# Performance work log

Measured on AMD Instinct MI355X. Metric: run time of the kernel, lower is better.

The kernel has to match this reference:

```python
import jax, jax.numpy as jnp
import numpy as np

N0, D, H, E0 = 50000, 128, 128, 800000
N1, E1, A, B, C = 20000, 320000, 100000, 64, 10


def _gcn(x, row, col, ew, n, W, b):
    # GCNConv: out = D^-1/2 (A + I) D^-1/2 (x W) + b, with edge weights
    xw = x @ W
    sl = jnp.arange(n)
    r = jnp.concatenate([row, sl])
    c = jnp.concatenate([col, sl])
    w = jnp.concatenate([ew, jnp.ones((n,), ew.dtype)])
    deg = jax.ops.segment_sum(w, c, num_segments=n)
    dinv = jax.lax.rsqrt(jnp.maximum(deg, 1e-12))
    norm = dinv[r] * w * dinv[c]
    return jax.ops.segment_sum(norm[:, None] * xw[r], c, num_segments=n) + b


def _block(x, row, col, ew, n, W1, b1, W2, b2, Wl, bl):
    # Block with num_inner_layers=2, jumping_knowledge='cat'
    x1 = jax.nn.relu(_gcn(x, row, col, ew, n, W1, b1))
    x2 = jax.nn.relu(_gcn(x1, row, col, ew, n, W2, b2))
    return jnp.concatenate([x1, x2], axis=1) @ Wl + bl


def _seg_max(x, idx, n):
    m = jax.ops.segment_max(x, idx, num_segments=n)
    return jnp.where(jnp.isfinite(m), m, 0.0)  # empty segments -> 0 like scatter_max default


def _lin_init(k, i, o):
    s = 1.0 / np.sqrt(i)
    return jax.random.uniform(k, (i, o), jnp.float32, -s, s)


def setup_inputs() -> dict:
    key = jax.random.key(0)
    ks = jax.random.split(key, 20)
    x = jax.random.normal(ks[0], (N0, D), jnp.float32)
    edge_index0 = jax.random.randint(ks[1], (2, E0), 0, N0)
    edge_weight0 = jax.random.uniform(ks[2], (E0,), jnp.float32)
    batch0 = jnp.sort(jax.random.randint(ks[3], (N0,), 0, B))
    cover_row = jax.random.randint(ks[4], (A,), 0, N0)
    cover_col = jnp.concatenate([jnp.arange(N1), jax.random.randint(ks[5], (A - N1,), 0, N1)])
    edge_index1 = jax.random.randint(ks[6], (2, E1), 0, N1)
    edge_weight1 = jax.random.uniform(ks[7], (E1,), jnp.float32)
    batch1 = jnp.sort(jax.random.randint(ks[8], (N1,), 0, B))
    params = dict(
        w_in1=_lin_init(ks[9], D, H), b_in1=jnp.zeros((H,), jnp.float32),
        w_in2=_lin_init(ks[10], H, H), b_in2=jnp.zeros((H,), jnp.float32),
        w_in_lin=_lin_init(ks[11], 2 * H, H), b_in_lin=jnp.zeros((H,), jnp.float32),
        w_b1=_lin_init(ks[12], 2 * H, H), b_b1=jnp.zeros((H,), jnp.float32),
        w_b2=_lin_init(ks[13], H, H), b_b2=jnp.zeros((H,), jnp.float32),
        w_b_lin=_lin_init(ks[14], 2 * H, H), b_b_lin=jnp.zeros((H,), jnp.float32),
        bn_gamma=jnp.ones((4 * H,), jnp.float32), bn_beta=jnp.zeros((4 * H,), jnp.float32),
        w_l1=_lin_init(ks[15], 4 * H, H), b_l1=jnp.zeros((H,), jnp.float32),
        w_l2=_lin_init(ks[16], H, C), b_l2=jnp.zeros((C,), jnp.float32),
    )
    return dict(x=x, edge_index0=edge_index0, edge_weight0=edge_weight0, batch0=batch0,
                cover_row=cover_row, cover_col=cover_col, edge_index1=edge_index1,
                edge_weight1=edge_weight1, batch1=batch1, **params)


def reference(x, edge_index0, edge_weight0, batch0, cover_row, cover_col,
              edge_index1, edge_weight1, batch1,
              w_in1, b_in1, w_in2, b_in2, w_in_lin, b_in_lin,
              w_b1, b_b1, w_b2, b_b2, w_b_lin, b_b_lin,
              bn_gamma, bn_beta, w_l1, b_l1, w_l2, b_l2):
    r0, c0 = edge_index0[0], edge_index0[1]
    h = jax.nn.relu(_block(x, r0, c0, edge_weight0, N0, w_in1, b_in1, w_in2, b_in2, w_in_lin, b_in_lin))
    xs = [jax.ops.segment_sum(h, batch0, num_segments=B), _seg_max(h, batch0, B)]
    # cover_pool_node: add + max over k-plex cover assignments
    hg = h[cover_row]
    h2 = jnp.concatenate([jax.ops.segment_sum(hg, cover_col, num_segments=N1),
                          _seg_max(hg, cover_col, N1)], axis=1)
    r1, c1 = edge_index1[0], edge_index1[1]
    h2 = jax.nn.relu(_block(h2, r1, c1, edge_weight1, N1, w_b1, b_b1, w_b2, b_b2, w_b_lin, b_b_lin))
    xs.append(jax.ops.segment_sum(h2, batch1, num_segments=B))
    xs.append(_seg_max(h2, batch1, B))
    z = jnp.concatenate(xs, axis=1)  # [B, 4H]
    # BatchNorm1d in eval mode: running stats (mean=0, var=1), eps=1e-5
    z = z * (bn_gamma * jax.lax.rsqrt(jnp.asarray(1.0 + 1e-5, z.dtype))) + bn_beta
    z = jax.nn.relu(z @ w_l1 + b_l1)
    logits = z @ w_l2 + b_l2  # dropout skipped (eval mode)
    return jax.nn.softmax(logits, axis=-1)
```

## Files before the change

### kernel.cpp

```cpp
#include <hip/hip_runtime.h>
#include <cmath>

#define HF 128
#define EPB 2048

namespace {

typedef __attribute__((ext_vector_type(8))) short short8;
typedef __attribute__((ext_vector_type(4))) float f32x4;

inline int cdiv(int a, int b) { return (a + b - 1) / b; }

__device__ inline unsigned short f2bf(float x) {
    unsigned u = __float_as_uint(x);
    return (unsigned short)((u + 0x7fffu + ((u >> 16) & 1u)) >> 16);
}
__device__ inline float bf2f(unsigned short u) {
    return __uint_as_float((unsigned)u << 16);
}
__device__ inline float bflo(unsigned v) { return __uint_as_float(v << 16); }
__device__ inline float bfhi(unsigned v) { return __uint_as_float(v & 0xffff0000u); }

#define FIXS 4194304.0f
#define FIXINV 2.384185791015625e-07f
#define SUMMASK ((1ULL << 40) - 1)

template <int K, bool AF32>
__device__ __forceinline__ void gemm_dev(int bid, const void* __restrict__ A1v, int lda1,
                                         const void* __restrict__ A2v, int lda2,
                                         const unsigned short* __restrict__ wpk,
                                         const float* __restrict__ bias, int relu,
                                         unsigned short* __restrict__ out, int N) {
    const int t = threadIdx.x;
    const int wv = t >> 6, lane = t & 63;
    const int l15 = lane & 15, lhi = lane >> 4;
    const int rbase = bid * 128 + wv * 32;

    f32x4 acc[2][8];
#pragma unroll
    for (int i = 0; i < 2; ++i)
#pragma unroll
        for (int g = 0; g < 8; ++g) acc[i][g] = {0.f, 0.f, 0.f, 0.f};

    int r[2];
#pragma unroll
    for (int ri = 0; ri < 2; ++ri) {
        int rr = rbase + ri * 16 + l15;
        r[ri] = (rr < N) ? rr : (N - 1);
    }

    for (int kc = 0; kc < K / 32; ++kc) {
        int kb = kc * 32 + lhi * 8;
        short8 a[2];
#pragma unroll
        for (int ri = 0; ri < 2; ++ri) {
            if (AF32) {
                const float* A = (const float*)A1v;
                const float* p = A + (size_t)r[ri] * lda1 + kb;
                float4 f0 = *reinterpret_cast<const float4*>(p);
                float4 f1 = *reinterpret_cast<const float4*>(p + 4);
                a[ri][0] = (short)f2bf(f0.x); a[ri][1] = (short)f2bf(f0.y);
                a[ri][2] = (short)f2bf(f0.z); a[ri][3] = (short)f2bf(f0.w);
                a[ri][4] = (short)f2bf(f1.x); a[ri][5] = (short)f2bf(f1.y);
                a[ri][6] = (short)f2bf(f1.z); a[ri][7] = (short)f2bf(f1.w);
            } else {
                const unsigned short* base;
                int kk, ld;
                if (K == 256 && kb >= 128) { base = (const unsigned short*)A2v; kk = kb - 128; ld = lda2; }
                else                       { base = (const unsigned short*)A1v; kk = kb;       ld = lda1; }
                a[ri] = *reinterpret_cast<const short8*>(base + (size_t)r[ri] * ld + kk);
            }
        }
        const unsigned short* wb = wpk + (size_t)(kc * 8) * 512 + lane * 8;
#pragma unroll
        for (int g = 0; g < 8; ++g) {
            short8 b = *reinterpret_cast<const short8*>(wb + (size_t)g * 512);
            acc[0][g] = __builtin_amdgcn_mfma_f32_16x16x32_bf16(a[0], b, acc[0][g], 0, 0, 0);
            acc[1][g] = __builtin_amdgcn_mfma_f32_16x16x32_bf16(a[1], b, acc[1][g], 0, 0, 0);
        }
    }

#pragma unroll
    for (int ri = 0; ri < 2; ++ri) {
#pragma unroll
        for (int g = 0; g < 8; ++g) {
            int col = l15 + g * 16;
            float bb = bias ? bias[col] : 0.f;
#pragma unroll
            for (int e = 0; e < 4; ++e) {
                int rr = rbase + ri * 16 + lhi * 4 + e;
                if (rr < N) {
                    float v = acc[ri][g][e] + bb;
                    if (relu) v = fmaxf(v, 0.f);
                    out[(size_t)rr * 128 + col] = f2bf(v);
                }
            }
        }
    }
}

template <int K, bool AF32>
__global__ void k_mfma_gemm(const void* __restrict__ A1v, int lda1,
                            const void* __restrict__ A2v, int lda2,
                            const unsigned short* __restrict__ wpk,
                            const float* __restrict__ bias, int relu,
                            unsigned short* __restrict__ out, int N) {
    gemm_dev<K, AF32>(blockIdx.x, A1v, lda1, A2v, lda2, wpk, bias, relu, out, N);
}

__device__ __forceinline__ void hist_dev(int e, int E, const int* __restrict__ col,
                                         const float* __restrict__ ew,
                                         unsigned long long* __restrict__ dc,
                                         unsigned* __restrict__ rank) {
    if (e < E) {
        unsigned long long v = (1ULL << 40) | (unsigned long long)(ew[e] * FIXS + 0.5f);
        unsigned long long old = atomicAdd(&dc[col[e]], v);
        rank[e] = (unsigned)(old >> 40);
    }
}

__device__ inline void scan256(int* s, int v, int gid, int n, int* __restrict__ excl,
                               int* __restrict__ partial, int pb) {
    s[threadIdx.x] = v;
    __syncthreads();
    for (int off = 1; off < 256; off <<= 1) {
        int t = (threadIdx.x >= off) ? s[threadIdx.x - off] : 0;
        __syncthreads();
        s[threadIdx.x] += t;
        __syncthreads();
    }
    if (gid < n) excl[gid] = s[threadIdx.x] - v;
    if (threadIdx.x == 255) partial[pb] = s[255];
}

__device__ __forceinline__ void fill_dev(int b, int t, const int* __restrict__ row,
                                         const int* __restrict__ col, const float* __restrict__ ew,
                                         const unsigned* __restrict__ rank,
                                         const float* __restrict__ dinv, const int* __restrict__ rp,
                                         int2* __restrict__ ed, int E, int Nn) {
    int xcd = b & 7, chunk = b >> 3;
    int lo = (int)((long long)Nn * xcd >> 3), hi = (int)((long long)Nn * (xcd + 1) >> 3);
    int base = chunk * EPB;
#pragma unroll
    for (int i = 0; i < EPB; i += 256) {
        int e = base + i + t;
        if (e < E) {
            int c = col[e];
            if (c >= lo && c < hi) {
                int r = row[e];
                ed[rp[c] + rank[e]] = make_int2(r, __float_as_int(ew[e] * dinv[r] * dinv[c]));
            }
        }
    }
}

__device__ __forceinline__ void gather_dev(int b, const unsigned* __restrict__ xw, int n,
                                           const int* __restrict__ rp, const int2* __restrict__ ed,
                                           const float* __restrict__ dinv,
                                           const float* __restrict__ bias,
                                           unsigned* __restrict__ out) {
    int wid = (b * 256 + (int)threadIdx.x) >> 6;
    if (wid >= n) return;
    int lane = threadIdx.x & 63;
    int s = rp[wid], e = rp[wid + 1];
    float d = dinv[wid];
    unsigned v = xw[(size_t)wid * 64 + lane];
    float ax = bflo(v) * d * d, ay = bfhi(v) * d * d;
    float bx = 0.f, by = 0.f, cx = 0.f, cy = 0.f, dx = 0.f, dy = 0.f;
    int i = s;
    for (; i + 4 <= e; i += 4) {
        unsigned long long p0 = __builtin_nontemporal_load((const unsigned long long*)(ed + i));
        unsigned long long p1 = __builtin_nontemporal_load((const unsigned long long*)(ed + i + 1));
        unsigned long long p2 = __builtin_nontemporal_load((const unsigned long long*)(ed + i + 2));
        unsigned long long p3 = __builtin_nontemporal_load((const unsigned long long*)(ed + i + 3));
        unsigned v0 = xw[(size_t)(unsigned)(p0 & 0xffffffffu) * 64 + lane];
        unsigned v1 = xw[(size_t)(unsigned)(p1 & 0xffffffffu) * 64 + lane];
        unsigned v2 = xw[(size_t)(unsigned)(p2 & 0xffffffffu) * 64 + lane];
        unsigned v3 = xw[(size_t)(unsigned)(p3 & 0xffffffffu) * 64 + lane];
        float c0 = __uint_as_float((unsigned)(p0 >> 32));
        float c1 = __uint_as_float((unsigned)(p1 >> 32));
        float c2 = __uint_as_float((unsigned)(p2 >> 32));
        float c3 = __uint_as_float((unsigned)(p3 >> 32));
        ax += c0 * bflo(v0); ay += c0 * bfhi(v0);
        bx += c1 * bflo(v1); by += c1 * bfhi(v1);
        cx += c2 * bflo(v2); cy += c2 * bfhi(v2);
        dx += c3 * bflo(v3); dy += c3 * bfhi(v3);
    }
    for (; i < e; ++i) {
        unsigned long long p0 = __builtin_nontemporal_load((const unsigned long long*)(ed + i));
        unsigned v0 = xw[(size_t)(unsigned)(p0 & 0xffffffffu) * 64 + lane];
        float c0 = __uint_as_float((unsigned)(p0 >> 32));
        ax += c0 * bflo(v0); ay += c0 * bfhi(v0);
    }
    ax += bx + cx + dx;
    ay += by + cy + dy;
    float2 bb = *reinterpret_cast<const float2*>(bias + lane * 2);
    ax = fmaxf(ax + bb.x, 0.f);
    ay = fmaxf(ay + bb.y, 0.f);
    out[(size_t)wid * 64 + lane] = (unsigned)f2bf(ax) | ((unsigned)f2bf(ay) << 16);
}

__global__ void k_prep0(const float* __restrict__ w0, const float* __restrict__ w1,
                        const float* __restrict__ w2, const float* __restrict__ w3,
                        const float* __restrict__ w4, const float* __restrict__ w5,
                        unsigned short* __restrict__ wpk,
                        const int* __restrict__ b0, int n0, const int* __restrict__ b1,
                        int n1, int B, int* __restrict__ bst0, int* __restrict__ bst1) {
    int b = blockIdx.x, t = threadIdx.x;
    if (b < 576) {
        int idx = b * 256 + t;
        const float* src; int local;
        if      (idx < 16384)  { src = w0; local = idx; }
        else if (idx < 32768)  { src = w1; local = idx - 16384; }
        else if (idx < 65536)  { src = w2; local = idx - 32768; }
        else if (idx < 98304)  { src = w3; local = idx - 65536; }
        else if (idx < 114688) { src = w4; local = idx - 98304; }
        else                   { src = w5; local = idx - 114688; }
        int e = local & 7, lane = (local >> 3) & 63, g = (local >> 9) & 7, kc = local >> 12;
        int colw = (lane & 15) + 16 * g;
        int k = kc * 32 + ((lane >> 4) << 3) + e;
        wpk[idx] = f2bf(src[k * 128 + colw]);
        return;
    }
    int idx = t;
    if (idx < 2 * (B + 1)) {
        int which = idx > B;
        int bb = which ? idx - (B + 1) : idx;
        const int* arr = which ? b1 : b0;
        int lo = 0, hi = which ? n1 : n0;
        while (lo < hi) {
            int mid = (lo + hi) >> 1;
            if (arr[mid] < bb) lo = mid + 1; else hi = mid;
        }
        (which ? bst1 : bst0)[bb] = lo;
    }
}

__global__ void k_prep1(const float* __restrict__ x, const unsigned short* __restrict__ wpk,
                        unsigned short* __restrict__ xw, int N0gemm, int nbG,
                        const int* __restrict__ col0, const float* __restrict__ ew0,
                        unsigned long long* __restrict__ dc0, unsigned* __restrict__ rank0,
                        int E0) {
    int b = blockIdx.x;
    if (b < nbG) {
        gemm_dev<128, true>(b, x, 128, nullptr, 0, wpk, nullptr, 0, xw, N0gemm);
        return;
    }
    b -= nbG;
    hist_dev(b * 256 + (int)threadIdx.x, E0, col0, ew0, dc0, rank0);
}

__global__ void k_scanA(const unsigned long long* __restrict__ dc0, int* __restrict__ rp0,
                        int* __restrict__ part0, float* __restrict__ dinv0, int n0) {
    __shared__ int s[256];
    int gid = blockIdx.x * 256 + threadIdx.x;
    int v = (gid < n0) ? (int)(dc0[gid] >> 40) : 0;
    scan256(s, v, gid, n0, rp0, part0, blockIdx.x);
    if (gid < n0) dinv0[gid] = rsqrtf(1.0f + (float)(dc0[gid] & SUMMASK) * FIXINV);
}

__global__ void k_scan2a(int* __restrict__ p0, int nb0) {
    __shared__ int s[256];
    int v = (threadIdx.x < nb0) ? p0[threadIdx.x] : 0;
    s[threadIdx.x] = v;
    __syncthreads();
    for (int off = 1; off < 256; off <<= 1) {
        int t = (threadIdx.x >= off) ? s[threadIdx.x - off] : 0;
        __syncthreads();
        s[threadIdx.x] += t;
        __syncthreads();
    }
    if (threadIdx.x < nb0) p0[threadIdx.x] = s[threadIdx.x] - v;
}

__global__ void k_scan3a(int* __restrict__ rp0, const int* __restrict__ part0, int n0, int tot) {
    int gid = blockIdx.x * 256 + threadIdx.x;
    if (gid < n0) rp0[gid] += part0[blockIdx.x];
    if (gid == 0) rp0[n0] = tot;
}

__global__ void k_fill0(const int* __restrict__ row0, const int* __restrict__ col0,
                        const float* __restrict__ ew0, const unsigned* __restrict__ rank0,
                        const float* __restrict__ dinv0, const int* __restrict__ rp0,
                        int2* __restrict__ ed0, int E0, int N0n) {
    fill_dev(blockIdx.x, threadIdx.x, row0, col0, ew0, rank0, dinv0, rp0, ed0, E0, N0n);
}

__global__ void k_gather_hist(const unsigned* __restrict__ xw, int n,
                              const int* __restrict__ rp, const int2* __restrict__ ed,
                              const float* __restrict__ dinv, const float* __restrict__ bias,
                              unsigned* __restrict__ out, int G,
                              const int* __restrict__ col1, const float* __restrict__ ew1,
                              unsigned long long* __restrict__ dc1, unsigned* __restrict__ rank1,
                              int E1, int nb1,
                              const int* __restrict__ ccol, int* __restrict__ ccnt,
                              unsigned* __restrict__ rankc, int A) {
    int b = blockIdx.x;
    if (b < G) { gather_dev(b, xw, n, rp, ed, dinv, bias, out); return; }
    b -= G;
    int t = threadIdx.x;
    if (b < nb1) { hist_dev(b * 256 + t, E1, col1, ew1, dc1, rank1); return; }
    b -= nb1;
    int e = b * 256 + t;
    if (e < A) rankc[e] = (unsigned)atomicAdd(&ccnt[ccol[e]], 1);
}

__global__ void k_gemm_scan(const void* __restrict__ A1v, const unsigned short* __restrict__ wpk,
                            unsigned short* __restrict__ out, int N, int nbG,
                            const unsigned long long* __restrict__ dc1, int* __restrict__ rp1,
                            int* __restrict__ part1, float* __restrict__ dinv1, int n1, int nbs1,
                            const int* __restrict__ ccnt, int* __restrict__ crp,
                            int* __restrict__ cpart, int nc) {
    __shared__ int s[256];
    int b = blockIdx.x;
    if (b < nbG) {
        gemm_dev<128, false>(b, A1v, 128, nullptr, 0, wpk, nullptr, 0, out, N);
        return;
    }
    b -= nbG;
    if (b < nbs1) {
        int gid = b * 256 + threadIdx.x;
        int v = (gid < n1) ? (int)(dc1[gid] >> 40) : 0;
        scan256(s, v, gid, n1, rp1, part1, b);
        if (gid < n1) dinv1[gid] = rsqrtf(1.0f + (float)(dc1[gid] & SUMMASK) * FIXINV);
        return;
    }
    b -= nbs1;
    {
        int gid = b * 256 + threadIdx.x;
        int v = (gid < nc) ? ccnt[gid] : 0;
        scan256(s, v, gid, nc, crp, cpart, b);
    }
}

__global__ void k_scan2b(int* __restrict__ p1, int nb1, int* __restrict__ p2, int nb2) {
    __shared__ int s[256];
    int* p = (blockIdx.x == 0) ? p1 : p2;
    int nb = (blockIdx.x == 0) ? nb1 : nb2;
    int v = (threadIdx.x < nb) ? p[threadIdx.x] : 0;
    s[threadIdx.x] = v;
    __syncthreads();
    for (int off = 1; off < 256; off <<= 1) {
        int t = (threadIdx.x >= off) ? s[threadIdx.x - off] : 0;
        __syncthreads();
        s[threadIdx.x] += t;
        __syncthreads();
    }
    if (threadIdx.x < nb) p[threadIdx.x] = s[threadIdx.x] - v;
}

__global__ void k_scan3b(int* __restrict__ rp1, const int* __restrict__ part1, int n1, int tot1,
                         int nb1, int* __restrict__ crp, const int* __restrict__ cpart,
                         int nc, int totc) {
    int b = blockIdx.x, t = threadIdx.x;
    if (b < nb1) {
        int gid = b * 256 + t;
        if (gid < n1) rp1[gid] += part1[b];
        if (gid == 0) rp1[n1] = tot1;
        return;
    }
    b -= nb1;
    int gid = b * 256 + t;
    if (gid < nc) crp[gid] += cpart[b];
    if (gid == 0) crp[nc] = totc;
}

__global__ void k_gather_fill(const unsigned* __restrict__ xw, int n,
                              const int* __restrict__ rp, const int2* __restrict__ ed,
                              const float* __restrict__ dinv, const float* __restrict__ bias,
                              unsigned* __restrict__ out, int G,
                              const int* __restrict__ row1, const int* __restrict__ col1,
                              const float* __restrict__ ew1, const unsigned* __restrict__ rank1,
                              const float* __restrict__ dinv1, const int* __restrict__ rp1,
                              int2* __restrict__ ed1, int E1, int N1n, int g1b,
                              const int* __restrict__ crow, const int* __restrict__ ccol,
                              const unsigned* __restrict__ rankc, const int* __restrict__ crp,
                              int* __restrict__ csrcs, int A) {
    int b = blockIdx.x, t = threadIdx.x;
    if (b < G) { gather_dev(b, xw, n, rp, ed, dinv, bias, out); return; }
    b -= G;
    if (b < g1b) { fill_dev(b, t, row1, col1, ew1, rank1, dinv1, rp1, ed1, E1, N1n); return; }
    b -= g1b;
    {
        int xcd = b & 7, chunk = b >> 3;
        int lo = (int)((long long)N1n * xcd >> 3), hi = (int)((long long)N1n * (xcd + 1) >> 3);
        int base = chunk * EPB;
#pragma unroll
        for (int i = 0; i < EPB; i += 256) {
            int e = base + i + t;
            if (e < A) {
                int c = ccol[e];
                if (c >= lo && c < hi) csrcs[crp[c] + rankc[e]] = crow[e];
            }
        }
    }
}

__global__ void k_gather(const unsigned* __restrict__ xw, int n, const int* __restrict__ rp,
                         const int2* __restrict__ ed, const float* __restrict__ dinv,
                         const float* __restrict__ bias, unsigned* __restrict__ out) {
    gather_dev(blockIdx.x, xw, n, rp, ed, dinv, bias, out);
}

__global__ void k_pool_cover(const unsigned short* __restrict__ h, const int* __restrict__ bst,
                             float* __restrict__ psum, float* __restrict__ pmax, int nsplit,
                             int nbpool, const unsigned* __restrict__ h32,
                             const int* __restrict__ crp, const int* __restrict__ csrcs,
                             unsigned* __restrict__ h2, int n1) {
    int t = threadIdx.x;
    if ((int)blockIdx.x < nbpool) {
        int blk = blockIdx.x;
        int b = blk / nsplit, sub = (blk % nsplit) * 2 + (t >> 7);
        int col = t & 127;
        int r0 = bst[b], r1 = bst[b + 1];
        float sum = 0.f, mx = 0.f;
        for (int r = r0 + sub; r < r1; r += 2 * nsplit) {
            float v = bf2f(h[(size_t)r * HF + col]);
            sum += v;
            mx = fmaxf(mx, v);
        }
        atomicAdd(&psum[b * HF + col], sum);
        atomicMax(reinterpret_cast<int*>(&pmax[b * HF + col]), __float_as_int(mx));
        return;
    }
    int wid = (((int)blockIdx.x - nbpool) * 256 + t) >> 6;
    if (wid >= n1) return;
    int lane = t & 63;
    int s = crp[wid], e = crp[wid + 1];
    float sx = 0.f, sy = 0.f, mx = 0.f, my = 0.f;
    for (int i = s; i < e; ++i) {
        unsigned v = h32[(size_t)csrcs[i] * 64 + lane];
        float vx = bflo(v), vy = bfhi(v);
        sx += vx; sy += vy;
        mx = fmaxf(mx, vx); my = fmaxf(my, vy);
    }
    h2[(size_t)wid * 128 + lane]      = (unsigned)f2bf(sx) | ((unsigned)f2bf(sy) << 16);
    h2[(size_t)wid * 128 + 64 + lane] = (unsigned)f2bf(mx) | ((unsigned)f2bf(my) << 16);
}

__global__ void k_pool256(const unsigned short* __restrict__ h, const int* __restrict__ bst,
                          float* __restrict__ psum, float* __restrict__ pmax, int nsplit) {
    int t = threadIdx.x;
    int blk = blockIdx.x;
    int b = blk / nsplit, sub = (blk % nsplit) * 2 + (t >> 7);
    int col = t & 127;
    int r0 = bst[b], r1 = bst[b + 1];
    float sum = 0.f, mx = 0.f;
    for (int r = r0 + sub; r < r1; r += 2 * nsplit) {
        float v = bf2f(h[(size_t)r * HF + col]);
        sum += v;
        mx = fmaxf(mx, v);
    }
    atomicAdd(&psum[b * HF + col], sum);
    atomicMax(reinterpret_cast<int*>(&pmax[b * HF + col]), __float_as_int(mx));
}

__global__ void k_head(const float* __restrict__ p0s, const float* __restrict__ p0m,
                       const float* __restrict__ p1s, const float* __restrict__ p1m,
                       const float* __restrict__ gamma, const float* __restrict__ beta,
                       const float* __restrict__ w1, const float* __restrict__ b1,
                       const float* __restrict__ w2, const float* __restrict__ b2,
                       float* __restrict__ out) {
    __shared__ float z[512];
    __shared__ float z1[128];
    __shared__ float lg[10];
    int b = blockIdx.x, t = threadIdx.x;
    const float s = rsqrtf(1.0f + 1e-5f);
    z[t]       = p0s[b * 128 + t] * (gamma[t] * s)       + beta[t];
    z[128 + t] = p0m[b * 128 + t] * (gamma[128 + t] * s) + beta[128 + t];
    z[256 + t] = p1s[b * 128 + t] * (gamma[256 + t] * s) + beta[256 + t];
    z[384 + t] = p1m[b * 128 + t] * (gamma[384 + t] * s) + beta[384 + t];
    __syncthreads();
    float acc = b1[t];
    for (int k = 0; k < 512; ++k) acc += z[k] * w1[k * 128 + t];
    z1[t] = fmaxf(acc, 0.f);
    __syncthreads();
    if (t < 10) {
        float a2 = b2[t];
        for (int k = 0; k < 128; ++k) a2 += z1[k] * w2[k * 10 + t];
        lg[t] = a2;
    }
    __syncthreads();
    if (t == 0) {
        float m = lg[0];
        for (int c = 1; c < 10; ++c) m = fmaxf(m, lg[c]);
        float e[10], ssum = 0.f;
        for (int c = 0; c < 10; ++c) { e[c] = expf(lg[c] - m); ssum += e[c]; }
        for (int c = 0; c < 10; ++c) out[b * 10 + c] = e[c] / ssum;
    }
}

}

extern "C" void kernel_launch(void* const* d_in, const int* in_sizes, int n_in,
                              void* d_out, int out_size, void* d_ws, size_t ws_size,
                              hipStream_t stream) {
    const float* x      = (const float*)d_in[0];
    const int*   ei0    = (const int*)d_in[1];
    const float* ew0    = (const float*)d_in[2];
    const int*   batch0 = (const int*)d_in[3];
    const int*   crow   = (const int*)d_in[4];
    const int*   ccol   = (const int*)d_in[5];
    const int*   ei1    = (const int*)d_in[6];
    const float* ew1    = (const float*)d_in[7];
    const int*   batch1 = (const int*)d_in[8];
    const float* w_in1  = (const float*)d_in[9];
    const float* b_in1  = (const float*)d_in[10];
    const float* w_in2  = (const float*)d_in[11];
    const float* b_in2  = (const float*)d_in[12];
    const float* w_inl  = (const float*)d_in[13];
    const float* b_inl  = (const float*)d_in[14];
    const float* w_b1   = (const float*)d_in[15];
    const float* b_b1   = (const float*)d_in[16];
    const float* w_b2   = (const float*)d_in[17];
    const float* b_b2   = (const float*)d_in[18];
    const float* w_bl   = (const float*)d_in[19];
    const float* b_bl   = (const float*)d_in[20];
    const float* gamma  = (const float*)d_in[21];
    const float* beta   = (const float*)d_in[22];
    const float* w_l1   = (const float*)d_in[23];
    const float* b_l1   = (const float*)d_in[24];
    const float* w_l2   = (const float*)d_in[25];
    const float* b_l2   = (const float*)d_in[26];

    const int N0 = in_sizes[0] / 128;
    const int E0 = in_sizes[2];
    const int A  = in_sizes[4];
    const int E1 = in_sizes[7];
    const int N1 = in_sizes[8];
    const int B  = out_size / 10;

    const int* row0 = ei0;
    const int* col0 = ei0 + E0;
    const int* row1 = ei1;
    const int* col1 = ei1 + E1;

    char* wsp = (char*)d_ws;
    size_t off = 0;
    auto alloc = [&](size_t bytes) -> char* {
        char* p = wsp + off;
        off += (bytes + 255) & ~(size_t)255;
        return p;
    };
    unsigned long long* dc0 = (unsigned long long*)alloc((size_t)N0 * 8);
    unsigned long long* dc1 = (unsigned long long*)alloc((size_t)N1 * 8);
    int*   ccnt  = (int*)alloc((size_t)N1 * 4);
    float* p0s   = (float*)alloc((size_t)B * HF * 4 * 4);
    float* p0m   = p0s + (size_t)B * HF;
    float* p1s   = p0m + (size_t)B * HF;
    float* p1m   = p1s + (size_t)B * HF;
    size_t zero_bytes = off;

    unsigned* xw  = (unsigned*)alloc((size_t)N0 * 64 * 4);
    unsigned* x1  = (unsigned*)alloc((size_t)N0 * 64 * 4);
    unsigned* x2  = (unsigned*)alloc((size_t)N0 * 64 * 4);
    unsigned* h   = (unsigned*)alloc((size_t)N0 * 64 * 4);
    unsigned* h2  = (unsigned*)alloc((size_t)N1 * 128 * 4);
    unsigned short* wpk = (unsigned short*)alloc(147456 * 2);
    float* dinv0 = (float*)alloc((size_t)N0 * 4);
    float* dinv1 = (float*)alloc((size_t)N1 * 4);
    int*   rp0   = (int*)alloc(((size_t)N0 + 1) * 4);
    int*   rp1   = (int*)alloc(((size_t)N1 + 1) * 4);
    int*   crp   = (int*)alloc(((size_t)N1 + 1) * 4);
    int*   part0 = (int*)alloc(256 * 4);
    int*   part1 = (int*)alloc(256 * 4);
    int*   cpart = (int*)alloc(256 * 4);
    int2*  ed0   = (int2*)alloc((size_t)E0 * 8);
    int2*  ed1   = (int2*)alloc((size_t)E1 * 8);
    int*   csrcs = (int*)alloc((size_t)A * 4);
    unsigned* rank0 = (unsigned*)alloc((size_t)E0 * 4);
    unsigned* rank1 = (unsigned*)alloc((size_t)E1 * 4);
    unsigned* rankc = (unsigned*)alloc((size_t)A * 4);
    int*   bst0  = (int*)alloc((size_t)(B + 1) * 4);
    int*   bst1  = (int*)alloc((size_t)(B + 1) * 4);
    (void)ws_size; (void)n_in;

    const int NSPLIT = 16;
    const int nbG0 = cdiv(N0, 128), nbG1 = cdiv(N1, 128);
    const int nbE0 = cdiv(E0, 256), nbE1 = cdiv(E1, 256), nbC = cdiv(A, 256);
    const int nbs0 = cdiv(N0, 256), nbs1 = cdiv(N1, 256), nbsc = cdiv(N1, 256);
    const int g1f = cdiv(E1, EPB) * 8, gcf = cdiv(A, EPB) * 8, g0f = cdiv(E0, EPB) * 8;
    const int G0 = cdiv(N0, 4), G1 = cdiv(N1, 4);

    hipMemsetAsync(dc0, 0, zero_bytes, stream);

    k_prep0<<<577, 256, 0, stream>>>(w_in1, w_in2, w_inl, w_b1, w_b2, w_bl, wpk,
                                     batch0, N0, batch1, N1, B, bst0, bst1);

    k_prep1<<<nbG0 + nbE0, 256, 0, stream>>>(x, wpk, (unsigned short*)xw, N0, nbG0,
                                             col0, ew0, dc0, rank0, E0);

    k_scanA<<<nbs0, 256, 0, stream>>>(dc0, rp0, part0, dinv0, N0);
    k_scan2a<<<1, 256, 0, stream>>>(part0, nbs0);
    k_scan3a<<<nbs0, 256, 0, stream>>>(rp0, part0, N0, E0);
    k_fill0<<<g0f, 256, 0, stream>>>(row0, col0, ew0, rank0, dinv0, rp0, ed0, E0, N0);

    k_gather_hist<<<G0 + nbE1 + nbC, 256, 0, stream>>>(
        xw, N0, rp0, ed0, dinv0, b_in1, x1, G0,
        col1, ew1, dc1, rank1, E1, nbE1, ccol, ccnt, rankc, A);

    k_gemm_scan<<<nbG0 + nbs1 + nbsc, 256, 0, stream>>>(
        x1, wpk + 16384, (unsigned short*)xw, N0, nbG0,
        dc1, rp1, part1, dinv1, N1, nbs1, ccnt, crp, cpart, N1);

    k_scan2b<<<2, 256, 0, stream>>>(part1, nbs1, cpart, nbsc);
    k_scan3b<<<nbs1 + nbsc, 256, 0, stream>>>(rp1, part1, N1, E1, nbs1, crp, cpart, N1, A);

    k_gather_fill<<<G0 + g1f + gcf, 256, 0, stream>>>(
        xw, N0, rp0, ed0, dinv0, b_in2, x2, G0,
        row1, col1, ew1, rank1, dinv1, rp1, ed1, E1, N1, g1f,
        crow, ccol, rankc, crp, csrcs, A);

    k_mfma_gemm<256, false><<<nbG0, 256, 0, stream>>>(
        x1, 128, (const unsigned short*)x2, 128, wpk + 32768, b_inl, 1,
        (unsigned short*)h, N0);

    k_pool_cover<<<B * NSPLIT + cdiv(N1, 4), 256, 0, stream>>>(
        (const unsigned short*)h, bst0, p0s, p0m, NSPLIT, B * NSPLIT,
        h, crp, csrcs, h2, N1);

    k_mfma_gemm<256, false><<<nbG1, 256, 0, stream>>>(
        h2, 256, (const unsigned short*)h2 + 128, 256, wpk + 65536, nullptr, 0,
        (unsigned short*)xw, N1);
    k_gather<<<G1, 256, 0, stream>>>(xw, N1, rp1, ed1, dinv1, b_b1, x1);
    k_mfma_gemm<128, false><<<nbG1, 256, 0, stream>>>(
        x1, 128, nullptr, 0, wpk + 98304, nullptr, 0, (unsigned short*)xw, N1);
    k_gather<<<G1, 256, 0, stream>>>(xw, N1, rp1, ed1, dinv1, b_b2, x2);
    k_mfma_gemm<256, false><<<nbG1, 256, 0, stream>>>(
        x1, 128, (const unsigned short*)x2, 128, wpk + 114688, b_bl, 1,
        (unsigned short*)h, N1);

    k_pool256<<<B * NSPLIT, 256, 0, stream>>>((const unsigned short*)h, bst1, p1s, p1m, NSPLIT);

    k_head<<<B, 128, 0, stream>>>(p0s, p0m, p1s, p1m, gamma, beta, w_l1, b_l1, w_l2, b_l2,
                                  (float*)d_out);
}
```

Before: 397.6 us.

## Pack CSR edge records into 32 bits with a 16-bit row and bf16 coefficient

```diff
diff --git a/kernel.cpp b/kernel.cpp
--- a/kernel.cpp
+++ b/kernel.cpp
@@ -8,6 +8,7 @@
 
 typedef __attribute__((ext_vector_type(8))) short short8;
 typedef __attribute__((ext_vector_type(4))) float f32x4;
+typedef unsigned long long u64;
 
 inline int cdiv(int a, int b) { return (a + b - 1) / b; }
 
@@ -110,11 +111,10 @@
 
 __device__ __forceinline__ void hist_dev(int e, int E, const int* __restrict__ col,
                                          const float* __restrict__ ew,
-                                         unsigned long long* __restrict__ dc,
-                                         unsigned* __restrict__ rank) {
+                                         u64* __restrict__ dc, unsigned* __restrict__ rank) {
     if (e < E) {
-        unsigned long long v = (1ULL << 40) | (unsigned long long)(ew[e] * FIXS + 0.5f);
-        unsigned long long old = atomicAdd(&dc[col[e]], v);
+        u64 v = (1ULL << 40) | (u64)(ew[e] * FIXS + 0.5f);
+        u64 old = atomicAdd(&dc[col[e]], v);
         rank[e] = (unsigned)(old >> 40);
     }
 }
@@ -137,7 +137,7 @@
                                          const int* __restrict__ col, const float* __restrict__ ew,
                                          const unsigned* __restrict__ rank,
                                          const float* __restrict__ dinv, const int* __restrict__ rp,
-                                         int2* __restrict__ ed, int E, int Nn) {
+                                         unsigned* __restrict__ ed, int E, int Nn) {
     int xcd = b & 7, chunk = b >> 3;
     int lo = (int)((long long)Nn * xcd >> 3), hi = (int)((long long)Nn * (xcd + 1) >> 3);
     int base = chunk * EPB;
@@ -148,14 +148,16 @@
             int c = col[e];
             if (c >= lo && c < hi) {
                 int r = row[e];
-                ed[rp[c] + rank[e]] = make_int2(r, __float_as_int(ew[e] * dinv[r] * dinv[c]));
+                ed[rp[c] + rank[e]] =
+                    (unsigned)r | ((unsigned)f2bf(ew[e] * dinv[r]) << 16);
             }
         }
     }
 }
 
 __device__ __forceinline__ void gather_dev(int b, const unsigned* __restrict__ xw, int n,
-                                           const int* __restrict__ rp, const int2* __restrict__ ed,
+                                           const int* __restrict__ rp,
+                                           const unsigned* __restrict__ ed,
                                            const float* __restrict__ dinv,
                                            const float* __restrict__ bias,
                                            unsigned* __restrict__ out) {
@@ -165,38 +167,38 @@
     int s = rp[wid], e = rp[wid + 1];
     float d = dinv[wid];
     unsigned v = xw[(size_t)wid * 64 + lane];
-    float ax = bflo(v) * d * d, ay = bfhi(v) * d * d;
+    float ax = bflo(v) * d, ay = bfhi(v) * d;
     float bx = 0.f, by = 0.f, cx = 0.f, cy = 0.f, dx = 0.f, dy = 0.f;
     int i = s;
+    for (; (i & 3) != 0 && i < e; ++i) {
+        unsigned q = ed[i];
+        unsigned v0 = xw[(size_t)(q & 0xffffu) * 64 + lane];
+        float c0 = bfhi(q);
+        ax += c0 * bflo(v0); ay += c0 * bfhi(v0);
+    }
     for (; i + 4 <= e; i += 4) {
-        unsigned long long p0 = __builtin_nontemporal_load((const unsigned long long*)(ed + i));
-        unsigned long long p1 = __builtin_nontemporal_load((const unsigned long long*)(ed + i + 1));
-        unsigned long long p2 = __builtin_nontemporal_load((const unsigned long long*)(ed + i + 2));
-        unsigned long long p3 = __builtin_nontemporal_load((const unsigned long long*)(ed + i + 3));
-        unsigned v0 = xw[(size_t)(unsigned)(p0 & 0xffffffffu) * 64 + lane];
-        unsigned v1 = xw[(size_t)(unsigned)(p1 & 0xffffffffu) * 64 + lane];
-        unsigned v2 = xw[(size_t)(unsigned)(p2 & 0xffffffffu) * 64 + lane];
-        unsigned v3 = xw[(size_t)(unsigned)(p3 & 0xffffffffu) * 64 + lane];
-        float c0 = __uint_as_float((unsigned)(p0 >> 32));
-        float c1 = __uint_as_float((unsigned)(p1 >> 32));
-        float c2 = __uint_as_float((unsigned)(p2 >> 32));
-        float c3 = __uint_as_float((unsigned)(p3 >> 32));
+        uint4 q = *reinterpret_cast<const uint4*>(ed + i);
+        unsigned v0 = xw[(size_t)(q.x & 0xffffu) * 64 + lane];
+        unsigned v1 = xw[(size_t)(q.y & 0xffffu) * 64 + lane];
+        unsigned v2 = xw[(size_t)(q.z & 0xffffu) * 64 + lane];
+        unsigned v3 = xw[(size_t)(q.w & 0xffffu) * 64 + lane];
+        float c0 = bfhi(q.x), c1 = bfhi(q.y), c2 = bfhi(q.z), c3 = bfhi(q.w);
         ax += c0 * bflo(v0); ay += c0 * bfhi(v0);
         bx += c1 * bflo(v1); by += c1 * bfhi(v1);
         cx += c2 * bflo(v2); cy += c2 * bfhi(v2);
         dx += c3 * bflo(v3); dy += c3 * bfhi(v3);
     }
     for (; i < e; ++i) {
-        unsigned long long p0 = __builtin_nontemporal_load((const unsigned long long*)(ed + i));
-        unsigned v0 = xw[(size_t)(unsigned)(p0 & 0xffffffffu) * 64 + lane];
-        float c0 = __uint_as_float((unsigned)(p0 >> 32));
+        unsigned q = ed[i];
+        unsigned v0 = xw[(size_t)(q & 0xffffu) * 64 + lane];
+        float c0 = bfhi(q);
         ax += c0 * bflo(v0); ay += c0 * bfhi(v0);
     }
     ax += bx + cx + dx;
     ay += by + cy + dy;
     float2 bb = *reinterpret_cast<const float2*>(bias + lane * 2);
-    ax = fmaxf(ax + bb.x, 0.f);
-    ay = fmaxf(ay + bb.y, 0.f);
+    ax = fmaxf(ax * d + bb.x, 0.f);
+    ay = fmaxf(ay * d + bb.y, 0.f);
     out[(size_t)wid * 64 + lane] = (unsigned)f2bf(ax) | ((unsigned)f2bf(ay) << 16);
 }
 
@@ -239,8 +241,7 @@
 __global__ void k_prep1(const float* __restrict__ x, const unsigned short* __restrict__ wpk,
                         unsigned short* __restrict__ xw, int N0gemm, int nbG,
                         const int* __restrict__ col0, const float* __restrict__ ew0,
-                        unsigned long long* __restrict__ dc0, unsigned* __restrict__ rank0,
-                        int E0) {
+                        u64* __restrict__ dc0, unsigned* __restrict__ rank0, int E0) {
     int b = blockIdx.x;
     if (b < nbG) {
         gemm_dev<128, true>(b, x, 128, nullptr, 0, wpk, nullptr, 0, xw, N0gemm);
@@ -250,7 +251,7 @@
     hist_dev(b * 256 + (int)threadIdx.x, E0, col0, ew0, dc0, rank0);
 }
 
-__global__ void k_scanA(const unsigned long long* __restrict__ dc0, int* __restrict__ rp0,
+__global__ void k_scanA(const u64* __restrict__ dc0, int* __restrict__ rp0,
                         int* __restrict__ part0, float* __restrict__ dinv0, int n0) {
     __shared__ int s[256];
     int gid = blockIdx.x * 256 + threadIdx.x;
@@ -282,16 +283,16 @@
 __global__ void k_fill0(const int* __restrict__ row0, const int* __restrict__ col0,
                         const float* __restrict__ ew0, const unsigned* __restrict__ rank0,
                         const float* __restrict__ dinv0, const int* __restrict__ rp0,
-                        int2* __restrict__ ed0, int E0, int N0n) {
+                        unsigned* __restrict__ ed0, int E0, int N0n) {
     fill_dev(blockIdx.x, threadIdx.x, row0, col0, ew0, rank0, dinv0, rp0, ed0, E0, N0n);
 }
 
 __global__ void k_gather_hist(const unsigned* __restrict__ xw, int n,
-                              const int* __restrict__ rp, const int2* __restrict__ ed,
+                              const int* __restrict__ rp, const unsigned* __restrict__ ed,
                               const float* __restrict__ dinv, const float* __restrict__ bias,
                               unsigned* __restrict__ out, int G,
                               const int* __restrict__ col1, const float* __restrict__ ew1,
-                              unsigned long long* __restrict__ dc1, unsigned* __restrict__ rank1,
+                              u64* __restrict__ dc1, unsigned* __restrict__ rank1,
                               int E1, int nb1,
                               const int* __restrict__ ccol, int* __restrict__ ccnt,
                               unsigned* __restrict__ rankc, int A) {
@@ -307,7 +308,7 @@
 
 __global__ void k_gemm_scan(const void* __restrict__ A1v, const unsigned short* __restrict__ wpk,
                             unsigned short* __restrict__ out, int N, int nbG,
-                            const unsigned long long* __restrict__ dc1, int* __restrict__ rp1,
+                            const u64* __restrict__ dc1, int* __restrict__ rp1,
                             int* __restrict__ part1, float* __restrict__ dinv1, int n1, int nbs1,
                             const int* __restrict__ ccnt, int* __restrict__ crp,
                             int* __restrict__ cpart, int nc) {
@@ -366,16 +367,16 @@
 }
 
 __global__ void k_gather_fill(const unsigned* __restrict__ xw, int n,
-                              const int* __restrict__ rp, const int2* __restrict__ ed,
+                              const int* __restrict__ rp, const unsigned* __restrict__ ed,
                               const float* __restrict__ dinv, const float* __restrict__ bias,
                               unsigned* __restrict__ out, int G,
                               const int* __restrict__ row1, const int* __restrict__ col1,
                               const float* __restrict__ ew1, const unsigned* __restrict__ rank1,
                               const float* __restrict__ dinv1, const int* __restrict__ rp1,
-                              int2* __restrict__ ed1, int E1, int N1n, int g1b,
+                              unsigned* __restrict__ ed1, int E1, int N1n, int g1b,
                               const int* __restrict__ crow, const int* __restrict__ ccol,
                               const unsigned* __restrict__ rankc, const int* __restrict__ crp,
-                              int* __restrict__ csrcs, int A) {
+                              unsigned short* __restrict__ csrcs, int A) {
     int b = blockIdx.x, t = threadIdx.x;
     if (b < G) { gather_dev(b, xw, n, rp, ed, dinv, bias, out); return; }
     b -= G;
@@ -390,14 +391,14 @@
             int e = base + i + t;
             if (e < A) {
                 int c = ccol[e];
-                if (c >= lo && c < hi) csrcs[crp[c] + rankc[e]] = crow[e];
+                if (c >= lo && c < hi) csrcs[crp[c] + rankc[e]] = (unsigned short)crow[e];
             }
         }
     }
 }
 
 __global__ void k_gather(const unsigned* __restrict__ xw, int n, const int* __restrict__ rp,
-                         const int2* __restrict__ ed, const float* __restrict__ dinv,
+                         const unsigned* __restrict__ ed, const float* __restrict__ dinv,
                          const float* __restrict__ bias, unsigned* __restrict__ out) {
     gather_dev(blockIdx.x, xw, n, rp, ed, dinv, bias, out);
 }
@@ -405,7 +406,8 @@
 __global__ void k_pool_cover(const unsigned short* __restrict__ h, const int* __restrict__ bst,
                              float* __restrict__ psum, float* __restrict__ pmax, int nsplit,
                              int nbpool, const unsigned* __restrict__ h32,
-                             const int* __restrict__ crp, const int* __restrict__ csrcs,
+                             const int* __restrict__ crp,
+                             const unsigned short* __restrict__ csrcs,
                              unsigned* __restrict__ h2, int n1) {
     int t = threadIdx.x;
     if ((int)blockIdx.x < nbpool) {
@@ -542,13 +544,13 @@
         off += (bytes + 255) & ~(size_t)255;
         return p;
     };
-    unsigned long long* dc0 = (unsigned long long*)alloc((size_t)N0 * 8);
-    unsigned long long* dc1 = (unsigned long long*)alloc((size_t)N1 * 8);
-    int*   ccnt  = (int*)alloc((size_t)N1 * 4);
-    float* p0s   = (float*)alloc((size_t)B * HF * 4 * 4);
-    float* p0m   = p0s + (size_t)B * HF;
-    float* p1s   = p0m + (size_t)B * HF;
-    float* p1m   = p1s + (size_t)B * HF;
+    u64*  dc0  = (u64*)alloc((size_t)N0 * 8);
+    u64*  dc1  = (u64*)alloc((size_t)N1 * 8);
+    int*  ccnt = (int*)alloc((size_t)N1 * 4);
+    float* p0s = (float*)alloc((size_t)B * HF * 4 * 4);
+    float* p0m = p0s + (size_t)B * HF;
+    float* p1s = p0m + (size_t)B * HF;
+    float* p1m = p1s + (size_t)B * HF;
     size_t zero_bytes = off;
 
     unsigned* xw  = (unsigned*)alloc((size_t)N0 * 64 * 4);
@@ -565,9 +567,9 @@
     int*   part0 = (int*)alloc(256 * 4);
     int*   part1 = (int*)alloc(256 * 4);
     int*   cpart = (int*)alloc(256 * 4);
-    int2*  ed0   = (int2*)alloc((size_t)E0 * 8);
-    int2*  ed1   = (int2*)alloc((size_t)E1 * 8);
-    int*   csrcs = (int*)alloc((size_t)A * 4);
+    unsigned* ed0 = (unsigned*)alloc((size_t)E0 * 4);
+    unsigned* ed1 = (unsigned*)alloc((size_t)E1 * 4);
+    unsigned short* csrcs = (unsigned short*)alloc((size_t)A * 2);
     unsigned* rank0 = (unsigned*)alloc((size_t)E0 * 4);
     unsigned* rank1 = (unsigned*)alloc((size_t)E1 * 4);
     unsigned* rankc = (unsigned*)alloc((size_t)A * 4);
@@ -575,11 +577,11 @@
     int*   bst1  = (int*)alloc((size_t)(B + 1) * 4);
     (void)ws_size; (void)n_in;
 
-    const int NSPLIT = 16;
+    const int NSPLIT = 4;
     const int nbG0 = cdiv(N0, 128), nbG1 = cdiv(N1, 128);
     const int nbE0 = cdiv(E0, 256), nbE1 = cdiv(E1, 256), nbC = cdiv(A, 256);
     const int nbs0 = cdiv(N0, 256), nbs1 = cdiv(N1, 256), nbsc = cdiv(N1, 256);
-    const int g1f = cdiv(E1, EPB) * 8, gcf = cdiv(A, EPB) * 8, g0f = cdiv(E0, EPB) * 8;
+    const int g0f = cdiv(E0, EPB) * 8, g1f = cdiv(E1, EPB) * 8, gcf = cdiv(A, EPB) * 8;
     const int G0 = cdiv(N0, 4), G1 = cdiv(N1, 4);
 
     hipMemsetAsync(dc0, 0, zero_bytes, stream);
```

After: 391.2 us. No clear change (-1.6%).
